# Performance work log

Measured on AMD Instinct MI355X. Metric: run time of the kernel, lower is better.

The kernel has to match this reference:

```python
import jax, jax.numpy as jnp
import numpy as np

NUM_HEADS = 6
HEAD_SIZE = 64
N_EMBD = 384


def setup_inputs() -> dict:
    key = jax.random.key(0)
    k1, k2, k3 = jax.random.split(key, 3)
    B, T, C = 256, 256, N_EMBD
    x = jax.random.normal(k1, (B, T, C), dtype=jnp.float32)
    # torch Linear(n_embd, 3*n_embd, bias=False): y = x @ W.T; store transposed for x @ W
    W_qkv = jax.random.normal(k2, (C, 3 * C), dtype=jnp.float32) * (1.0 / np.sqrt(C))
    W_proj = jax.random.normal(k3, (C, C), dtype=jnp.float32) * (1.0 / np.sqrt(C))
    b_proj = jnp.zeros((C,), dtype=jnp.float32)
    return {"x": x, "W_qkv": W_qkv, "W_proj": W_proj, "b_proj": b_proj}


def reference(x, W_qkv, W_proj, b_proj):
    B, T, C = x.shape
    H, D = NUM_HEADS, HEAD_SIZE
    qkv = x @ W_qkv                                  # [B, T, 3C]
    q, k, v = jnp.split(qkv, 3, axis=-1)
    # [B, T, C] -> [B, H, T, D]
    q = q.reshape(B, T, H, D).transpose(0, 2, 1, 3)
    k = k.reshape(B, T, H, D).transpose(0, 2, 1, 3)
    v = v.reshape(B, T, H, D).transpose(0, 2, 1, 3)
    att = jnp.einsum("bhtd,bhsd->bhts", q, k) / np.sqrt(D).astype(jnp.float32)
    causal = jnp.tril(jnp.ones((T, T), dtype=bool))  # tril buffer
    att = jnp.where(causal[None, None], att, -jnp.inf)
    att = jax.nn.softmax(att, axis=-1)
    # dropout layers are identity in eval mode
    out = jnp.einsum("bhts,bhsd->bhtd", att, v)      # [B, H, T, D]
    out = out.transpose(0, 2, 1, 3).reshape(B, T, C)
    return out @ W_proj.T @ jnp.eye(C, dtype=out.dtype) if False else out @ W_proj + b_proj
```

## Files before the change

### kernel.cpp

```cpp
#include <hip/hip_runtime.h>
#include <hip/hip_bf16.h>
#include <stdint.h>

typedef __hip_bfloat16 bf16;
using f32x4 = __attribute__((ext_vector_type(4))) float;
using s16x8 = __attribute__((ext_vector_type(8))) short;

#define MFMA16(A_, B_, C_) __builtin_amdgcn_mfma_f32_16x16x32_bf16((A_), (B_), (C_), 0, 0, 0)

__device__ __forceinline__ void gload16(const void* g, void* l) {
  __builtin_amdgcn_global_load_lds((const __attribute__((address_space(1))) void*)g,
                                   (__attribute__((address_space(3))) void*)l, 16, 0, 0);
}

__global__ __launch_bounds__(256) void detect_kernel(const void* __restrict__ x,
                                                     int* __restrict__ flag) {
  __shared__ int cnt;
  if (threadIdx.x == 0) cnt = 0;
  __syncthreads();
  const uint32_t* w = (const uint32_t*)x;
  int local = 0;
#pragma unroll
  for (int i = 0; i < 8; ++i) {
    uint32_t v = w[threadIdx.x * 8 + i];
    uint32_t e = (v >> 7) & 0xFF;
    if (e >= 110 && e <= 135) local++;
  }
  atomicAdd(&cnt, local);
  __syncthreads();
  if (threadIdx.x == 0) *flag = (cnt < 1024) ? 1 : 0;
}

__global__ __launch_bounds__(256) void convert_kernel(const void* __restrict__ x,
                                                      bf16* __restrict__ xb,
                                                      size_t elem_off,
                                                      const int* __restrict__ flag) {
  size_t i = ((size_t)blockIdx.x * 256 + threadIdx.x) * 8;
  if (*flag) {
    const float* xf = (const float*)x + elem_off + i;
    float4 a = ((const float4*)xf)[0];
    float4 b = ((const float4*)xf)[1];
    union { bf16 h[8]; uint4 u; } o;
    o.h[0] = __float2bfloat16(a.x); o.h[1] = __float2bfloat16(a.y);
    o.h[2] = __float2bfloat16(a.z); o.h[3] = __float2bfloat16(a.w);
    o.h[4] = __float2bfloat16(b.x); o.h[5] = __float2bfloat16(b.y);
    o.h[6] = __float2bfloat16(b.z); o.h[7] = __float2bfloat16(b.w);
    *(uint4*)(&xb[i]) = o.u;
  } else {
    *(uint4*)(&xb[i]) = *(const uint4*)((const bf16*)x + elem_off + i);
  }
}

__global__ __launch_bounds__(256) void transpose_kernel(const void* __restrict__ W,
                                                        bf16* __restrict__ Wt,
                                                        int K, int N,
                                                        const int* __restrict__ flag) {
  int idx = blockIdx.x * 256 + threadIdx.x;
  if (idx >= K * N) return;
  int n = idx / K;
  int k = idx - n * K;
  if (*flag)
    Wt[idx] = __float2bfloat16(((const float*)W)[k * N + n]);
  else
    Wt[idx] = ((const bf16*)W)[k * N + n];
}

template <int MODE>
__global__ __launch_bounds__(256) void gemm_kernel(
    const bf16* __restrict__ A, const bf16* __restrict__ Bt,
    bf16* __restrict__ qb, bf16* __restrict__ kb, bf16* __restrict__ vb,
    void* __restrict__ outp, const void* __restrict__ bias,
    int r_off, const int* __restrict__ flag) {
  constexpr int K = 384;
  __shared__ bf16 Ash[128 * 32];
  __shared__ bf16 Bsh[128 * 32];
  const int tid = threadIdx.x;
  const int lane = tid & 63;
  const int wave = tid >> 6;
  const int wm = wave & 1, wn = wave >> 1;
  const int l15 = lane & 15, quad = lane >> 4;
  const int n0 = blockIdx.x * 128, m0 = blockIdx.y * 128;

  const int rl = lane >> 2;
  const int slot = lane & 3;
  const int sc = (slot - (lane >> 3)) & 3;
  const size_t lane_goff = (size_t)rl * K + sc * 8;

  const int arow0 = wave * 32;
  const bf16* Ag0 = A + (size_t)(m0 + arow0) * K + lane_goff;
  const bf16* Ag1 = Ag0 + (size_t)16 * K;
  const bf16* Bg0 = Bt + (size_t)(n0 + arow0) * K + lane_goff;
  const bf16* Bg1 = Bg0 + (size_t)16 * K;
  bf16* Al0 = &Ash[arow0 * 32];
  bf16* Al1 = &Ash[(arow0 + 16) * 32];
  bf16* Bl0 = &Bsh[arow0 * 32];
  bf16* Bl1 = &Bsh[(arow0 + 16) * 32];

  const int fc = ((quad + (l15 >> 1)) & 3) * 8;

  const f32x4 z4 = {0.f, 0.f, 0.f, 0.f};
  f32x4 acc[4][4];
#pragma unroll
  for (int i = 0; i < 4; ++i)
#pragma unroll
    for (int j = 0; j < 4; ++j) acc[i][j] = z4;

  for (int kt = 0; kt < 12; ++kt) {
    const int k0 = kt * 32;
    gload16(Ag0 + k0, Al0);
    gload16(Ag1 + k0, Al1);
    gload16(Bg0 + k0, Bl0);
    gload16(Bg1 + k0, Bl1);
    __syncthreads();
    s16x8 af[4], bfr[4];
#pragma unroll
    for (int i = 0; i < 4; ++i) {
      af[i] = *(const s16x8*)(&Ash[(wm * 64 + i * 16 + l15) * 32 + fc]);
      bfr[i] = *(const s16x8*)(&Bsh[(wn * 64 + i * 16 + l15) * 32 + fc]);
    }
#pragma unroll
    for (int i = 0; i < 4; ++i)
#pragma unroll
      for (int j = 0; j < 4; ++j) acc[i][j] = MFMA16(af[i], bfr[j], acc[i][j]);
    __syncthreads();
  }

  const int mbase = m0 + wm * 64;
  const int nbase = n0 + wn * 64;
  if (MODE == 0) {
    const int sel = blockIdx.x / 3;
    bf16* dst = (sel == 0) ? qb : ((sel == 1) ? kb : vb);
#pragma unroll
    for (int i = 0; i < 4; ++i) {
#pragma unroll
      for (int j = 0; j < 4; ++j) {
        int n_g = nbase + j * 16 + l15;
        int c = n_g - sel * 384;
        int h = c >> 6, d = c & 63;
#pragma unroll
        for (int r = 0; r < 4; ++r) {
          int m_loc = mbase + i * 16 + quad * 4 + r;
          int b = m_loc >> 8, t = m_loc & 255;
          bf16 bv = __float2bfloat16(acc[i][j][r]);
          int bh = b * 6 + h;
          if (sel < 2) {
            dst[(size_t)bh * 16384 + t * 64 + d] = bv;
          } else {
            int rr = t & 31;
            int pos = (((rr & 15) >> 2) << 3) | (rr & 3) | ((rr >> 4) << 2);
            int tt = (t & ~31) | pos;
            dst[(size_t)bh * 16384 + d * 256 + tt] = bv;
          }
        }
      }
    }
  } else {
    const int f32io = *flag;
#pragma unroll
    for (int i = 0; i < 4; ++i) {
#pragma unroll
      for (int j = 0; j < 4; ++j) {
        int n_g = nbase + j * 16 + l15;
        float bsv = f32io ? ((const float*)bias)[n_g]
                          : __bfloat162float(((const bf16*)bias)[n_g]);
#pragma unroll
        for (int r = 0; r < 4; ++r) {
          int m_loc = mbase + i * 16 + quad * 4 + r;
          size_t o = (size_t)(r_off + m_loc) * 384 + n_g;
          float val = acc[i][j][r] + bsv;
          if (f32io)
            ((float*)outp)[o] = val;
          else
            ((bf16*)outp)[o] = __float2bfloat16(val);
        }
      }
    }
  }
}

__global__ __launch_bounds__(256, 3) void attn_kernel(const bf16* __restrict__ Q,
                                                      const bf16* __restrict__ Kb,
                                                      const bf16* __restrict__ Vt,
                                                      bf16* __restrict__ attn_out) {
  const int tid = threadIdx.x;
  const int lane = tid & 63;
  const int wave = tid >> 6;
  const int l15 = lane & 15, quad = lane >> 4;
  const int nblk = gridDim.x;
  int blk = blockIdx.x;
  if ((nblk & 7) == 0)
    blk = (blockIdx.x & 7) * (nblk >> 3) + (blockIdx.x >> 3);
  const int p = blk & 1;
  const int bh = blk >> 1;
  const int jA = p * 4 + wave;
  const int jB = 15 - jA;
  const size_t base = (size_t)bh * 16384;
  const int q0A = jA * 16, q0B = jB * 16;

  s16x8 qA0 = *(const s16x8*)(&Q[base + (q0A + l15) * 64 + quad * 8]);
  s16x8 qA1 = *(const s16x8*)(&Q[base + (q0A + l15) * 64 + 32 + quad * 8]);
  s16x8 qB0 = *(const s16x8*)(&Q[base + (q0B + l15) * 64 + quad * 8]);
  s16x8 qB1 = *(const s16x8*)(&Q[base + (q0B + l15) * 64 + 32 + quad * 8]);

  const int ktA = (jA + 2) >> 1;
  const int ktB = (jB + 2) >> 1;
  const int tqA = q0A + l15, tqB = q0B + l15;
  const f32x4 z4 = {0.f, 0.f, 0.f, 0.f};

  const bf16* Kp = Kb + base + (size_t)l15 * 64 + quad * 8;
  const bf16* Vp = Vt + base + (size_t)l15 * 256 + quad * 8;

  typedef union { s16x8 v; uint32_t w[4]; } pf_t;

  s16x8 kf[3][4];
  s16x8 vf[2][4];
#pragma unroll
  for (int i = 0; i < 4; ++i) {
    kf[0][i] = *(const s16x8*)(Kp + (size_t)((i >> 1) * 16) * 64 + (i & 1) * 32);
    kf[1][i] = *(const s16x8*)(Kp + (size_t)(32 + (i >> 1) * 16) * 64 + (i & 1) * 32);
  }
#pragma unroll
  for (int dt = 0; dt < 4; ++dt) vf[0][dt] = *(const s16x8*)(Vp + (size_t)dt * 4096);

  f32x4 ofA[4], ofB[4];
#pragma unroll
  for (int dt = 0; dt < 4; ++dt) { ofA[dt] = z4; ofB[dt] = z4; }
  float rsA = 0.f, rsB = 0.f;

#pragma unroll
  for (int t = 0; t < 8; ++t) {
    if (t < ktB) {
      if (t + 2 < ktB) {
        const bf16* Kn = Kp + (size_t)(t + 2) * 32 * 64;
#pragma unroll
        for (int i = 0; i < 4; ++i)
          kf[(t + 2) % 3][i] = *(const s16x8*)(Kn + (size_t)((i >> 1) * 16) * 64 + (i & 1) * 32);
      }
      if (t + 1 < ktB) {
#pragma unroll
        for (int dt = 0; dt < 4; ++dt)
          vf[(t + 1) & 1][dt] = *(const s16x8*)(Vp + (size_t)dt * 4096 + (t + 1) * 32);
      }
      pf_t pfB;
#pragma unroll
      for (int hf = 0; hf < 2; ++hf) {
        const int nt = 2 * t + hf;
        if (nt <= jB) {
          f32x4 s = MFMA16(kf[t % 3][hf * 2 + 0], qB0, z4);
          s = MFMA16(kf[t % 3][hf * 2 + 1], qB1, s);
          const int tk0 = nt * 16 + quad * 4;
          float p0 = (tk0 + 0 <= tqB) ? __expf(s[0] * 0.125f) : 0.f;
          float p1 = (tk0 + 1 <= tqB) ? __expf(s[1] * 0.125f) : 0.f;
          float p2 = (tk0 + 2 <= tqB) ? __expf(s[2] * 0.125f) : 0.f;
          float p3 = (tk0 + 3 <= tqB) ? __expf(s[3] * 0.125f) : 0.f;
          rsB += (p0 + p1) + (p2 + p3);
          union { bf16 hh[2]; uint32_t u; } w0, w1;
          w0.hh[0] = __float2bfloat16(p0); w0.hh[1] = __float2bfloat16(p1);
          w1.hh[0] = __float2bfloat16(p2); w1.hh[1] = __float2bfloat16(p3);
          pfB.w[hf * 2 + 0] = w0.u;
          pfB.w[hf * 2 + 1] = w1.u;
        } else {
          pfB.w[hf * 2 + 0] = 0u;
          pfB.w[hf * 2 + 1] = 0u;
        }
      }
      if (t < ktA) {
        pf_t pfA;
#pragma unroll
        for (int hf = 0; hf < 2; ++hf) {
          const int nt = 2 * t + hf;
          if (nt <= jA) {
            f32x4 s = MFMA16(kf[t % 3][hf * 2 + 0], qA0, z4);
            s = MFMA16(kf[t % 3][hf * 2 + 1], qA1, s);
            const int tk0 = nt * 16 + quad * 4;
            float p0 = (tk0 + 0 <= tqA) ? __expf(s[0] * 0.125f) : 0.f;
            float p1 = (tk0 + 1 <= tqA) ? __expf(s[1] * 0.125f) : 0.f;
            float p2 = (tk0 + 2 <= tqA) ? __expf(s[2] * 0.125f) : 0.f;
            float p3 = (tk0 + 3 <= tqA) ? __expf(s[3] * 0.125f) : 0.f;
            rsA += (p0 + p1) + (p2 + p3);
            union { bf16 hh[2]; uint32_t u; } w0, w1;
            w0.hh[0] = __float2bfloat16(p0); w0.hh[1] = __float2bfloat16(p1);
            w1.hh[0] = __float2bfloat16(p2); w1.hh[1] = __float2bfloat16(p3);
            pfA.w[hf * 2 + 0] = w0.u;
            pfA.w[hf * 2 + 1] = w1.u;
          } else {
            pfA.w[hf * 2 + 0] = 0u;
            pfA.w[hf * 2 + 1] = 0u;
          }
        }
#pragma unroll
        for (int dt = 0; dt < 4; ++dt) ofA[dt] = MFMA16(vf[t & 1][dt], pfA.v, ofA[dt]);
      }
#pragma unroll
      for (int dt = 0; dt < 4; ++dt) ofB[dt] = MFMA16(vf[t & 1][dt], pfB.v, ofB[dt]);
    }
  }

  rsA += __shfl_xor(rsA, 16);
  rsA += __shfl_xor(rsA, 32);
  rsB += __shfl_xor(rsB, 16);
  rsB += __shfl_xor(rsB, 32);
  const float invA = 1.0f / rsA;
  const float invB = 1.0f / rsB;

  const int b = bh / 6;
  const int h = bh - b * 6;
  const size_t orowA = (size_t)(b * 256 + q0A + l15) * 384 + h * 64;
  const size_t orowB = (size_t)(b * 256 + q0B + l15) * 384 + h * 64;
#pragma unroll
  for (int dt = 0; dt < 4; ++dt) {
    union { bf16 h4[4]; uint2 u; } oa, ob;
#pragma unroll
    for (int r = 0; r < 4; ++r) {
      oa.h4[r] = __float2bfloat16(ofA[dt][r] * invA);
      ob.h4[r] = __float2bfloat16(ofB[dt][r] * invB);
    }
    *(uint2*)(&attn_out[orowA + dt * 16 + quad * 4]) = oa.u;
    *(uint2*)(&attn_out[orowB + dt * 16 + quad * 4]) = ob.u;
  }
}

extern "C" void kernel_launch(void* const* d_in, const int* in_sizes, int n_in,
                              void* d_out, int out_size, void* d_ws, size_t ws_size,
                              hipStream_t stream) {
  const void* x = d_in[0];
  const void* Wqkv = d_in[1];
  const void* Wproj = d_in[2];
  const void* bproj = d_in[3];

  char* ws = (char*)d_ws;
  int* flag = (int*)ws;                ws += 256;
  bf16* Wt_qkv = (bf16*)ws;            ws += (size_t)1152 * 384 * 2;
  bf16* Wt_proj = (bf16*)ws;           ws += (size_t)384 * 384 * 2;

  const size_t per_batch = (size_t)5 * 98304 * 2;
  size_t used = (size_t)(ws - (char*)d_ws);
  size_t remain = (ws_size > used) ? (ws_size - used) : 0;
  int NB = (int)(remain / per_batch);
  if (NB > 256) NB = 256;
  if (NB < 1) NB = 1;

  bf16* xb_buf = (bf16*)ws;
  bf16* q_buf = xb_buf + (size_t)NB * 98304;
  bf16* k_buf = q_buf + (size_t)NB * 98304;
  bf16* vt_buf = k_buf + (size_t)NB * 98304;
  bf16* attn_buf = vt_buf + (size_t)NB * 98304;

  detect_kernel<<<1, 256, 0, stream>>>(x, flag);
  transpose_kernel<<<(384 * 1152 + 255) / 256, 256, 0, stream>>>(Wqkv, Wt_qkv, 384, 1152, flag);
  transpose_kernel<<<(384 * 384 + 255) / 256, 256, 0, stream>>>(Wproj, Wt_proj, 384, 384, flag);

  for (int b0 = 0; b0 < 256; b0 += NB) {
    int nb = (256 - b0 < NB) ? (256 - b0) : NB;
    int r_off = b0 * 256;
    convert_kernel<<<nb * 48, 256, 0, stream>>>(x, xb_buf, (size_t)r_off * 384, flag);
    gemm_kernel<0><<<dim3(9, 2 * nb), 256, 0, stream>>>(
        xb_buf, Wt_qkv, q_buf, k_buf, vt_buf, nullptr, nullptr, 0, flag);
    attn_kernel<<<nb * 12, 256, 0, stream>>>(q_buf, k_buf, vt_buf, attn_buf);
    gemm_kernel<1><<<dim3(3, 2 * nb), 256, 0, stream>>>(
        attn_buf, Wt_proj, nullptr, nullptr, nullptr, d_out, bproj, r_off, flag);
  }
}
```

Before: 457.2 us.

## Restructure GEMM to keep full-K A strip in LDS and stream B from global

The GEMM kernel now loads an entire 64-row by 384-K strip of A into shared memory once per block, then loops over every output column tile. B fragments are read directly from global memory into registers. This removes the per-k-step LDS staging and the barriers of the old 128x128 tiled loop, and it reuses A across all N tiles. In exchange, B reuse drops and B traffic relies on cache hits. The grid becomes one-dimensional over row strips.

```diff
diff --git a/kernel.cpp b/kernel.cpp
--- a/kernel.cpp
+++ b/kernel.cpp
@@ -72,106 +72,95 @@
     void* __restrict__ outp, const void* __restrict__ bias,
     int r_off, const int* __restrict__ flag) {
   constexpr int K = 384;
-  __shared__ bf16 Ash[128 * 32];
-  __shared__ bf16 Bsh[128 * 32];
+  constexpr int NT = (MODE == 0) ? 9 : 3;
+  __shared__ bf16 Ash[12][64 * 32];
   const int tid = threadIdx.x;
   const int lane = tid & 63;
   const int wave = tid >> 6;
-  const int wm = wave & 1, wn = wave >> 1;
   const int l15 = lane & 15, quad = lane >> 4;
-  const int n0 = blockIdx.x * 128, m0 = blockIdx.y * 128;
+  const int m0 = blockIdx.x * 64;
 
   const int rl = lane >> 2;
   const int slot = lane & 3;
   const int sc = (slot - (lane >> 3)) & 3;
-  const size_t lane_goff = (size_t)rl * K + sc * 8;
-
-  const int arow0 = wave * 32;
-  const bf16* Ag0 = A + (size_t)(m0 + arow0) * K + lane_goff;
-  const bf16* Ag1 = Ag0 + (size_t)16 * K;
-  const bf16* Bg0 = Bt + (size_t)(n0 + arow0) * K + lane_goff;
-  const bf16* Bg1 = Bg0 + (size_t)16 * K;
-  bf16* Al0 = &Ash[arow0 * 32];
-  bf16* Al1 = &Ash[(arow0 + 16) * 32];
-  bf16* Bl0 = &Bsh[arow0 * 32];
-  bf16* Bl1 = &Bsh[(arow0 + 16) * 32];
+
+  const bf16* Ag = A + (size_t)(m0 + wave * 16 + rl) * K + sc * 8;
+#pragma unroll
+  for (int kt = 0; kt < 12; ++kt) gload16(Ag + kt * 32, &Ash[kt][wave * 512]);
+  __syncthreads();
 
   const int fc = ((quad + (l15 >> 1)) & 3) * 8;
-
   const f32x4 z4 = {0.f, 0.f, 0.f, 0.f};
-  f32x4 acc[4][4];
-#pragma unroll
-  for (int i = 0; i < 4; ++i)
-#pragma unroll
-    for (int j = 0; j < 4; ++j) acc[i][j] = z4;
-
-  for (int kt = 0; kt < 12; ++kt) {
-    const int k0 = kt * 32;
-    gload16(Ag0 + k0, Al0);
-    gload16(Ag1 + k0, Al1);
-    gload16(Bg0 + k0, Bl0);
-    gload16(Bg1 + k0, Bl1);
-    __syncthreads();
-    s16x8 af[4], bfr[4];
-#pragma unroll
-    for (int i = 0; i < 4; ++i) {
-      af[i] = *(const s16x8*)(&Ash[(wm * 64 + i * 16 + l15) * 32 + fc]);
-      bfr[i] = *(const s16x8*)(&Bsh[(wn * 64 + i * 16 + l15) * 32 + fc]);
+
+  for (int nt = 0; nt < NT; ++nt) {
+    f32x4 acc[4][2];
+#pragma unroll
+    for (int i = 0; i < 4; ++i)
+#pragma unroll
+      for (int j = 0; j < 2; ++j) acc[i][j] = z4;
+
+    const bf16* Bg = Bt + (size_t)(nt * 128 + wave * 32 + l15) * K + quad * 8;
+#pragma unroll
+    for (int kt = 0; kt < 12; ++kt) {
+      s16x8 af[4], bfr[2];
+#pragma unroll
+      for (int i = 0; i < 4; ++i)
+        af[i] = *(const s16x8*)(&Ash[kt][(i * 16 + l15) * 32 + fc]);
+#pragma unroll
+      for (int j = 0; j < 2; ++j)
+        bfr[j] = *(const s16x8*)(Bg + (size_t)j * 16 * K + kt * 32);
+#pragma unroll
+      for (int i = 0; i < 4; ++i)
+#pragma unroll
+        for (int j = 0; j < 2; ++j) acc[i][j] = MFMA16(af[i], bfr[j], acc[i][j]);
     }
-#pragma unroll
-    for (int i = 0; i < 4; ++i)
-#pragma unroll
-      for (int j = 0; j < 4; ++j) acc[i][j] = MFMA16(af[i], bfr[j], acc[i][j]);
-    __syncthreads();
-  }
-
-  const int mbase = m0 + wm * 64;
-  const int nbase = n0 + wn * 64;
-  if (MODE == 0) {
-    const int sel = blockIdx.x / 3;
-    bf16* dst = (sel == 0) ? qb : ((sel == 1) ? kb : vb);
-#pragma unroll
-    for (int i = 0; i < 4; ++i) {
-#pragma unroll
-      for (int j = 0; j < 4; ++j) {
-        int n_g = nbase + j * 16 + l15;
+
+    if (MODE == 0) {
+      const int sel = nt / 3;
+      bf16* dst = (sel == 0) ? qb : ((sel == 1) ? kb : vb);
+#pragma unroll
+      for (int j = 0; j < 2; ++j) {
+        int n_g = nt * 128 + wave * 32 + j * 16 + l15;
         int c = n_g - sel * 384;
         int h = c >> 6, d = c & 63;
 #pragma unroll
-        for (int r = 0; r < 4; ++r) {
-          int m_loc = mbase + i * 16 + quad * 4 + r;
-          int b = m_loc >> 8, t = m_loc & 255;
-          bf16 bv = __float2bfloat16(acc[i][j][r]);
-          int bh = b * 6 + h;
-          if (sel < 2) {
-            dst[(size_t)bh * 16384 + t * 64 + d] = bv;
-          } else {
-            int rr = t & 31;
-            int pos = (((rr & 15) >> 2) << 3) | (rr & 3) | ((rr >> 4) << 2);
-            int tt = (t & ~31) | pos;
-            dst[(size_t)bh * 16384 + d * 256 + tt] = bv;
+        for (int i = 0; i < 4; ++i) {
+#pragma unroll
+          for (int r = 0; r < 4; ++r) {
+            int m_loc = m0 + i * 16 + quad * 4 + r;
+            int b = m_loc >> 8, t = m_loc & 255;
+            bf16 bv = __float2bfloat16(acc[i][j][r]);
+            int bh = b * 6 + h;
+            if (sel < 2) {
+              dst[(size_t)bh * 16384 + t * 64 + d] = bv;
+            } else {
+              int rr = t & 31;
+              int pos = (((rr & 15) >> 2) << 3) | (rr & 3) | ((rr >> 4) << 2);
+              int tt = (t & ~31) | pos;
+              dst[(size_t)bh * 16384 + d * 256 + tt] = bv;
+            }
           }
         }
       }
-    }
-  } else {
-    const int f32io = *flag;
-#pragma unroll
-    for (int i = 0; i < 4; ++i) {
-#pragma unroll
-      for (int j = 0; j < 4; ++j) {
-        int n_g = nbase + j * 16 + l15;
+    } else {
+      const int f32io = *flag;
+#pragma unroll
+      for (int j = 0; j < 2; ++j) {
+        int n_g = nt * 128 + wave * 32 + j * 16 + l15;
         float bsv = f32io ? ((const float*)bias)[n_g]
                           : __bfloat162float(((const bf16*)bias)[n_g]);
 #pragma unroll
-        for (int r = 0; r < 4; ++r) {
-          int m_loc = mbase + i * 16 + quad * 4 + r;
-          size_t o = (size_t)(r_off + m_loc) * 384 + n_g;
-          float val = acc[i][j][r] + bsv;
-          if (f32io)
-            ((float*)outp)[o] = val;
-          else
-            ((bf16*)outp)[o] = __float2bfloat16(val);
+        for (int i = 0; i < 4; ++i) {
+#pragma unroll
+          for (int r = 0; r < 4; ++r) {
+            int m_loc = m0 + i * 16 + quad * 4 + r;
+            size_t o = (size_t)(r_off + m_loc) * 384 + n_g;
+            float val = acc[i][j][r] + bsv;
+            if (f32io)
+              ((float*)outp)[o] = val;
+            else
+              ((bf16*)outp)[o] = __float2bfloat16(val);
+          }
         }
       }
     }
@@ -354,10 +343,10 @@
     int nb = (256 - b0 < NB) ? (256 - b0) : NB;
     int r_off = b0 * 256;
     convert_kernel<<<nb * 48, 256, 0, stream>>>(x, xb_buf, (size_t)r_off * 384, flag);
-    gemm_kernel<0><<<dim3(9, 2 * nb), 256, 0, stream>>>(
+    gemm_kernel<0><<<dim3(4 * nb), 256, 0, stream>>>(
         xb_buf, Wt_qkv, q_buf, k_buf, vt_buf, nullptr, nullptr, 0, flag);
     attn_kernel<<<nb * 12, 256, 0, stream>>>(q_buf, k_buf, vt_buf, attn_buf);
-    gemm_kernel<1><<<dim3(3, 2 * nb), 256, 0, stream>>>(
+    gemm_kernel<1><<<dim3(4 * nb), 256, 0, stream>>>(
         attn_buf, Wt_proj, nullptr, nullptr, nullptr, d_out, bproj, r_off, flag);
   }
 }
```

After: 514.0 us. +12.4%, slower.
